# Optimization experiments

Measured on AMD Instinct MI355X. Metric: run time of the kernel, lower is better.

The kernel has to match this reference:

```python
import jax, jax.numpy as jnp
import numpy as np

N_NODES = 100000


def gcn_conv(x, src, dst, W, b, n_nodes):
    """PyG GCNConv: out = D^{-1/2} (A + I) D^{-1/2} (x @ W) + b.
    src/dst are the original (non-self-loop) edges; self loops handled analytically.
    """
    h = x @ W  # [N, out]
    ones = jnp.ones(src.shape[0], dtype=h.dtype)
    # degree including self loop
    deg = jax.ops.segment_sum(ones, dst, num_segments=n_nodes) + 1.0  # [N]
    dinv = jax.lax.rsqrt(deg)
    norm = dinv[src] * dinv[dst]  # [E]
    msg = h[src] * norm[:, None]  # gather + scale
    agg = jax.ops.segment_sum(msg, dst, num_segments=n_nodes)  # scatter-add
    # self-loop contribution: norm = deg^{-1/2} * deg^{-1/2} = 1/deg
    agg = agg + h * (1.0 / deg)[:, None]
    return agg + b


def setup_inputs() -> dict:
    key = jax.random.key(0)
    k1, k2, k3, k4 = jax.random.split(key, 4)
    n, e = N_NODES, 3200000
    x = jax.random.normal(k1, (n, 256), dtype=jnp.float32)
    edge_index = jax.random.randint(k2, (2, e), 0, n, dtype=jnp.int64)
    W1 = jax.random.normal(k3, (256, 64), dtype=jnp.float32) * (1.0 / np.sqrt(256))
    b1 = jnp.zeros((64,), dtype=jnp.float32)
    W2 = jax.random.normal(k4, (64, 4), dtype=jnp.float32) * (1.0 / np.sqrt(64))
    b2 = jnp.zeros((4,), dtype=jnp.float32)
    return {"x": x, "edge_index": edge_index, "W1": W1, "b1": b1, "W2": W2, "b2": b2}


def reference(x, edge_index, W1, b1, W2, b2):
    n = x.shape[0]
    src, dst = edge_index[0], edge_index[1]
    h = gcn_conv(x, src, dst, W1, b1, n)
    h = jax.nn.leaky_relu(h, negative_slope=0.01)  # nn.LeakyReLU default
    # F.dropout in eval mode is identity
    h = gcn_conv(h, src, dst, W2, b2, n)
    return jax.nn.softmax(h, axis=1)
```

## Files before the change

### kernel.cpp

```cpp
#include <hip/hip_runtime.h>
#include <hip/hip_bf16.h>
#include <math.h>


#define NB 512
#define MAXB 512
#define SCHUNK 6400

typedef __attribute__((ext_vector_type(8))) short bf16x8;
typedef __attribute__((ext_vector_type(4))) float f32x4;

__device__ __forceinline__ int edge_val(const void* ep, size_t idx, int is64) {
    if (is64) return (int)(((const long long*)ep)[idx]);
    return ((const int*)ep)[idx];
}

__device__ __forceinline__ unsigned short f2bf(float f) {
    unsigned int u = __float_as_uint(f);
    return (unsigned short)((u + 0x7FFFu + ((u >> 16) & 1u)) >> 16);
}
__device__ __forceinline__ float bf2f(unsigned short b) {
    return __uint_as_float((unsigned int)b << 16);
}

__global__ void detect_width(const unsigned int* __restrict__ ew, int* __restrict__ flag) {
    if (threadIdx.x == 0 && blockIdx.x == 0) {
        int f = 1;
        for (int i = 0; i < 64; ++i)
            if (ew[2 * i + 1] != 0u) { f = 0; break; }
        *flag = f;
    }
}

__global__ __launch_bounds__(256) void hist_pass(
    const void* __restrict__ edges, int E, const int* __restrict__ flagp,
    int* __restrict__ ghist, int B) {
    __shared__ int hist[MAXB];
    const int tid = threadIdx.x;
    for (int i = tid; i < B; i += 256) hist[i] = 0;
    __syncthreads();
    const int is64 = *flagp;
    const int per = (E + NB - 1) / NB;
    const int s0 = blockIdx.x * per;
    const int s1 = min(s0 + per, E);
    for (int i = s0 + tid; i < s1; i += 256) {
        const int d = edge_val(edges, (size_t)E + i, is64);
        atomicAdd(&hist[d >> 8], 1);
    }
    __syncthreads();
    for (int i = tid; i < B; i += 256) ghist[(size_t)blockIdx.x * B + i] = hist[i];
}

__global__ __launch_bounds__(NB) void col_scan(
    const int* __restrict__ ghist, int* __restrict__ goff,
    int* __restrict__ bsum, int B) {
    __shared__ int sm[NB];
    const int tid = threadIdx.x;
    const int b = blockIdx.x;
    const int v = ghist[(size_t)tid * B + b];
    sm[tid] = v;
    __syncthreads();
    for (int off = 1; off < NB; off <<= 1) {
        int val = (tid >= off) ? sm[tid - off] : 0;
        __syncthreads();
        sm[tid] += val;
        __syncthreads();
    }
    goff[(size_t)tid * B + b] = sm[tid] - v;
    if (tid == NB - 1) bsum[b] = sm[tid];
}

__global__ __launch_bounds__(512) void base_scan(
    const int* __restrict__ bsum, int* __restrict__ bbase,
    int* __restrict__ row_ptr, int B, int n, int E) {
    __shared__ int sm[512];
    const int tid = threadIdx.x;
    const int v = (tid < B) ? bsum[tid] : 0;
    sm[tid] = v;
    __syncthreads();
    for (int off = 1; off < 512; off <<= 1) {
        int val = (tid >= off) ? sm[tid - off] : 0;
        __syncthreads();
        sm[tid] += val;
        __syncthreads();
    }
    if (tid < B) bbase[tid] = sm[tid] - v;
    if (tid == 0) { bbase[B] = E; row_ptr[n] = E; }
}

__global__ __launch_bounds__(512) void scatter_pass(
    const void* __restrict__ edges, int E, const int* __restrict__ flagp,
    const int* __restrict__ ghist, const int* __restrict__ goff,
    const int* __restrict__ bbase, unsigned int* __restrict__ ebuf, int B) {
    __shared__ unsigned int buf[SCHUNK];
    __shared__ int lb[MAXB];
    __shared__ int lf[MAXB];
    __shared__ int sm[MAXB];
    const int tid = threadIdx.x;
    const int blk = blockIdx.x;
    const int is64 = *flagp;
    const int per = (E + NB - 1) / NB;
    const int s0 = blk * per;
    const int s1 = min(s0 + per, E);

    if (per <= SCHUNK) {
        const int c = (tid < B) ? ghist[(size_t)blk * B + tid] : 0;
        sm[tid] = c;
        __syncthreads();
        for (int off = 1; off < MAXB; off <<= 1) {
            int val = (tid >= off) ? sm[tid - off] : 0;
            __syncthreads();
            sm[tid] += val;
            __syncthreads();
        }
        if (tid < B) { lb[tid] = sm[tid] - c; lf[tid] = sm[tid] - c; }
        __syncthreads();
        for (int i = s0 + tid; i < s1; i += 512) {
            const int d = edge_val(edges, (size_t)E + i, is64);
            const int s = edge_val(edges, (size_t)i, is64);
            const unsigned int val = ((unsigned int)s << 8) | (unsigned int)(d & 255);
            const int pos = atomicAdd(&lf[d >> 8], 1);
            buf[pos] = val;
        }
        __syncthreads();
        const int lane = tid & 63;
        const int wv = tid >> 6;
        for (int b = wv; b < B; b += 8) {
            const int lo = lb[b];
            const int cnt = lf[b] - lo;
            if (cnt > 0) {
                unsigned int* dst = ebuf + bbase[b] + goff[(size_t)blk * B + b];
                for (int k = lane; k < cnt; k += 64) dst[k] = buf[lo + k];
            }
        }
    } else {
        for (int i = tid; i < B; i += 512)
            lf[i] = bbase[i] + goff[(size_t)blk * B + i];
        __syncthreads();
        for (int i = s0 + tid; i < s1; i += 512) {
            const int d = edge_val(edges, (size_t)E + i, is64);
            const int s = edge_val(edges, (size_t)i, is64);
            const int pos = atomicAdd(&lf[d >> 8], 1);
            ebuf[pos] = ((unsigned int)s << 8) | (unsigned int)(d & 255);
        }
    }
}

__global__ __launch_bounds__(512) void bucket_csr(
    const unsigned int* __restrict__ ebuf, const int* __restrict__ bbase,
    int* __restrict__ row_ptr, float* __restrict__ dinv,
    int* __restrict__ col_src, int n) {
    __shared__ int hist[256];
    __shared__ int scn[256];
    __shared__ int fill[256];
    const int tid = threadIdx.x;
    const int b = blockIdx.x;
    if (tid < 256) hist[tid] = 0;
    __syncthreads();
    const int base = bbase[b];
    const int m = bbase[b + 1] - base;
    const unsigned int* eb = ebuf + base;
    for (int i = tid; i < m; i += 512) atomicAdd(&hist[eb[i] & 255u], 1);
    __syncthreads();
    if (tid < 256) scn[tid] = hist[tid];
    __syncthreads();
    for (int off = 1; off < 256; off <<= 1) {
        int val = 0;
        if (tid < 256 && tid >= off) val = scn[tid - off];
        __syncthreads();
        if (tid < 256) scn[tid] += val;
        __syncthreads();
    }
    if (tid < 256) {
        const int excl = scn[tid] - hist[tid];
        fill[tid] = excl;
        const int v = b * 256 + tid;
        if (v < n) {
            row_ptr[v] = base + excl;
            dinv[v] = rsqrtf((float)hist[tid] + 1.0f);
        }
    }
    __syncthreads();
    for (int i = tid; i < m; i += 512) {
        const unsigned int e = eb[i];
        const int p = atomicAdd(&fill[e & 255u], 1);
        col_src[base + p] = (int)(e >> 8);
    }
}

__global__ __launch_bounds__(256) void gemm1_kernel(
    const float* __restrict__ x, const float* __restrict__ W1,
    const float* __restrict__ dinv, unsigned short* __restrict__ hs1b, int n) {
    __shared__ unsigned short wt[64 * 264];
    const int tid = threadIdx.x;
    for (int i = tid; i < 4096; i += 256) {
        const int k = i >> 4;
        const int c0 = (i & 15) * 4;
        const float4 w = *((const float4*)W1 + i);
        wt[(c0 + 0) * 264 + k] = f2bf(w.x);
        wt[(c0 + 1) * 264 + k] = f2bf(w.y);
        wt[(c0 + 2) * 264 + k] = f2bf(w.z);
        wt[(c0 + 3) * 264 + k] = f2bf(w.w);
    }
    __syncthreads();

    const int lane = tid & 63;
    const int wid = tid >> 6;
    const int row0 = blockIdx.x * 64 + wid * 16;
    const int rr = lane & 15;
    const int kh = lane >> 4;

    union FragU { bf16x8 v; unsigned short u[8]; };
    bf16x8 af[8];
    {
        int r = row0 + rr;
        if (r >= n) r = n - 1;
        const float* xr = x + (size_t)r * 256 + kh * 8;
#pragma unroll
        for (int ks = 0; ks < 8; ++ks) {
            const float4 p0 = *(const float4*)(xr + ks * 32);
            const float4 p1 = *(const float4*)(xr + ks * 32 + 4);
            FragU f;
            f.u[0] = f2bf(p0.x); f.u[1] = f2bf(p0.y);
            f.u[2] = f2bf(p0.z); f.u[3] = f2bf(p0.w);
            f.u[4] = f2bf(p1.x); f.u[5] = f2bf(p1.y);
            f.u[6] = f2bf(p1.z); f.u[7] = f2bf(p1.w);
            af[ks] = f.v;
        }
    }
    f32x4 acc[4];
#pragma unroll
    for (int ct = 0; ct < 4; ++ct) acc[ct] = (f32x4){0.f, 0.f, 0.f, 0.f};
#pragma unroll
    for (int ct = 0; ct < 4; ++ct) {
        const unsigned short* wcol = wt + (ct * 16 + rr) * 264 + kh * 8;
#pragma unroll
        for (int ks = 0; ks < 8; ++ks) {
            const bf16x8 bf = *(const bf16x8*)(wcol + ks * 32);
            acc[ct] = __builtin_amdgcn_mfma_f32_16x16x32_bf16(af[ks], bf, acc[ct], 0, 0, 0);
        }
    }
#pragma unroll
    for (int j = 0; j < 4; ++j) {
        const int gr = row0 + kh * 4 + j;
        if (gr < n) {
            const float dv = dinv[gr];
#pragma unroll
            for (int ct = 0; ct < 4; ++ct)
                hs1b[(size_t)gr * 64 + ct * 16 + rr] = f2bf(acc[ct][j] * dv);
        }
    }
}

__global__ __launch_bounds__(256) void agg1_kernel(
    const int* __restrict__ row_ptr, const int* __restrict__ col_src,
    const unsigned short* __restrict__ hs1b, const float* __restrict__ dinv,
    const float* __restrict__ b1, const float* __restrict__ W2,
    float* __restrict__ hs2, int n) {
    const int lane = threadIdx.x & 63;
    int v = blockIdx.x * 4 + (threadIdx.x >> 6);
    v = __builtin_amdgcn_readfirstlane(v);
    if (v >= n) return;
    const int g = lane >> 4;
    const int q = lane & 15;
    const int rs = row_ptr[v];
    const int re = row_ptr[v + 1];
    float a0 = 0.f, a1 = 0.f, a2 = 0.f, a3 = 0.f;
    float c0 = 0.f, c1 = 0.f, c2 = 0.f, c3 = 0.f;
    int e = rs;
    for (; e + 32 <= re; e += 32) {
        const int cs = col_src[e + (lane & 31)];
        const int s0 = __shfl(cs, 0 + g),  s1 = __shfl(cs, 4 + g);
        const int s2 = __shfl(cs, 8 + g),  s3 = __shfl(cs, 12 + g);
        const int s4 = __shfl(cs, 16 + g), s5 = __shfl(cs, 20 + g);
        const int s6 = __shfl(cs, 24 + g), s7 = __shfl(cs, 28 + g);
        const ushort4 r0 = *((const ushort4*)(hs1b + (size_t)s0 * 64) + q);
        const ushort4 r1 = *((const ushort4*)(hs1b + (size_t)s1 * 64) + q);
        const ushort4 r2 = *((const ushort4*)(hs1b + (size_t)s2 * 64) + q);
        const ushort4 r3 = *((const ushort4*)(hs1b + (size_t)s3 * 64) + q);
        const ushort4 r4 = *((const ushort4*)(hs1b + (size_t)s4 * 64) + q);
        const ushort4 r5 = *((const ushort4*)(hs1b + (size_t)s5 * 64) + q);
        const ushort4 r6 = *((const ushort4*)(hs1b + (size_t)s6 * 64) + q);
        const ushort4 r7 = *((const ushort4*)(hs1b + (size_t)s7 * 64) + q);
        a0 += bf2f(r0.x) + bf2f(r1.x) + bf2f(r2.x) + bf2f(r3.x);
        a1 += bf2f(r0.y) + bf2f(r1.y) + bf2f(r2.y) + bf2f(r3.y);
        a2 += bf2f(r0.z) + bf2f(r1.z) + bf2f(r2.z) + bf2f(r3.z);
        a3 += bf2f(r0.w) + bf2f(r1.w) + bf2f(r2.w) + bf2f(r3.w);
        c0 += bf2f(r4.x) + bf2f(r5.x) + bf2f(r6.x) + bf2f(r7.x);
        c1 += bf2f(r4.y) + bf2f(r5.y) + bf2f(r6.y) + bf2f(r7.y);
        c2 += bf2f(r4.z) + bf2f(r5.z) + bf2f(r6.z) + bf2f(r7.z);
        c3 += bf2f(r4.w) + bf2f(r5.w) + bf2f(r6.w) + bf2f(r7.w);
    }
    a0 += c0; a1 += c1; a2 += c2; a3 += c3;
    for (; e + 16 <= re; e += 16) {
        const int cs = col_src[e + q];
        const int s0 = __shfl(cs, 0 + g);
        const int s1 = __shfl(cs, 4 + g);
        const int s2 = __shfl(cs, 8 + g);
        const int s3 = __shfl(cs, 12 + g);
        const ushort4 r0 = *((const ushort4*)(hs1b + (size_t)s0 * 64) + q);
        const ushort4 r1 = *((const ushort4*)(hs1b + (size_t)s1 * 64) + q);
        const ushort4 r2 = *((const ushort4*)(hs1b + (size_t)s2 * 64) + q);
        const ushort4 r3 = *((const ushort4*)(hs1b + (size_t)s3 * 64) + q);
        a0 += bf2f(r0.x) + bf2f(r1.x) + bf2f(r2.x) + bf2f(r3.x);
        a1 += bf2f(r0.y) + bf2f(r1.y) + bf2f(r2.y) + bf2f(r3.y);
        a2 += bf2f(r0.z) + bf2f(r1.z) + bf2f(r2.z) + bf2f(r3.z);
        a3 += bf2f(r0.w) + bf2f(r1.w) + bf2f(r2.w) + bf2f(r3.w);
    }
    for (; e < re; e += 4) {
        if (e + g < re) {
            const int s = col_src[e + g];
            const ushort4 r = *((const ushort4*)(hs1b + (size_t)s * 64) + q);
            a0 += bf2f(r.x); a1 += bf2f(r.y); a2 += bf2f(r.z); a3 += bf2f(r.w);
        }
    }
    a0 += __shfl_xor(a0, 16); a1 += __shfl_xor(a1, 16);
    a2 += __shfl_xor(a2, 16); a3 += __shfl_xor(a3, 16);
    a0 += __shfl_xor(a0, 32); a1 += __shfl_xor(a1, 32);
    a2 += __shfl_xor(a2, 32); a3 += __shfl_xor(a3, 32);
    const ushort4 sr = *((const ushort4*)(hs1b + (size_t)v * 64) + q);
    const float dv = dinv[v];
    const float4 bb = *((const float4*)b1 + q);
    float4 res;
    res.x = dv * (a0 + bf2f(sr.x)) + bb.x;
    res.y = dv * (a1 + bf2f(sr.y)) + bb.y;
    res.z = dv * (a2 + bf2f(sr.z)) + bb.z;
    res.w = dv * (a3 + bf2f(sr.w)) + bb.w;
    res.x = res.x > 0.f ? res.x : 0.01f * res.x;
    res.y = res.y > 0.f ? res.y : 0.01f * res.y;
    res.z = res.z > 0.f ? res.z : 0.01f * res.z;
    res.w = res.w > 0.f ? res.w : 0.01f * res.w;
    const float4* W2v = (const float4*)W2;
    const float4 w0 = W2v[q * 4 + 0], w1 = W2v[q * 4 + 1];
    const float4 w2 = W2v[q * 4 + 2], w3 = W2v[q * 4 + 3];
    float4 p;
    p.x = res.x * w0.x + res.y * w1.x + res.z * w2.x + res.w * w3.x;
    p.y = res.x * w0.y + res.y * w1.y + res.z * w2.y + res.w * w3.y;
    p.z = res.x * w0.z + res.y * w1.z + res.z * w2.z + res.w * w3.z;
    p.w = res.x * w0.w + res.y * w1.w + res.z * w2.w + res.w * w3.w;
#pragma unroll
    for (int s = 1; s < 16; s <<= 1) {
        p.x += __shfl_xor(p.x, s); p.y += __shfl_xor(p.y, s);
        p.z += __shfl_xor(p.z, s); p.w += __shfl_xor(p.w, s);
    }
    if (lane == 0) {
        float4 o; o.x = p.x * dv; o.y = p.y * dv; o.z = p.z * dv; o.w = p.w * dv;
        *(float4*)(hs2 + (size_t)v * 4) = o;
    }
}

__global__ __launch_bounds__(256) void agg2_kernel(
    const int* __restrict__ row_ptr, const int* __restrict__ col_src,
    const float* __restrict__ hs2, const float* __restrict__ dinv,
    const float* __restrict__ b2, float* __restrict__ out, int n) {
    const int lane = threadIdx.x & 63;
    int v = blockIdx.x * 4 + (threadIdx.x >> 6);
    v = __builtin_amdgcn_readfirstlane(v);
    if (v >= n) return;
    const int c = lane & 3;
    const int ei = lane >> 2;
    const int rs = row_ptr[v];
    const int re = row_ptr[v + 1];
    float acc = 0.f;
    for (int e0 = rs; e0 < re; e0 += 16) {
        const int e = e0 + ei;
        if (e < re) {
            const int s = col_src[e];
            acc += hs2[(size_t)s * 4 + c];
        }
    }
    acc += __shfl_xor(acc, 4);
    acc += __shfl_xor(acc, 8);
    acc += __shfl_xor(acc, 16);
    acc += __shfl_xor(acc, 32);
    const float val = dinv[v] * (acc + hs2[(size_t)v * 4 + c]) + b2[c];
    float m = fmaxf(val, __shfl_xor(val, 1));
    m = fmaxf(m, __shfl_xor(m, 2));
    const float ex = __expf(val - m);
    float s = ex + __shfl_xor(ex, 1);
    s += __shfl_xor(s, 2);
    if (lane < 4) out[(size_t)v * 4 + c] = ex / s;
}

extern "C" void kernel_launch(void* const* d_in, const int* in_sizes, int n_in,
                              void* d_out, int out_size, void* d_ws, size_t ws_size,
                              hipStream_t stream) {
    const float* x  = (const float*)d_in[0];
    const void*  ei = d_in[1];
    const float* W1 = (const float*)d_in[2];
    const float* b1 = (const float*)d_in[3];
    const float* W2 = (const float*)d_in[4];
    const float* b2 = (const float*)d_in[5];
    const int n = in_sizes[0] / 256;
    const int E = in_sizes[1] / 2;
    const int B = (n + 255) / 256;

    char* ws = (char*)d_ws;
    size_t off = 0;
    auto alloc = [&](size_t bytes) -> void* {
        void* p = ws + off;
        off += (bytes + 255) & ~(size_t)255;
        return p;
    };
    int*   flag    = (int*)alloc(sizeof(int) * 64);
    int*   ghist   = (int*)alloc(sizeof(int) * (size_t)NB * B);
    int*   goff    = (int*)alloc(sizeof(int) * (size_t)NB * B);
    int*   bsum    = (int*)alloc(sizeof(int) * B);
    int*   bbase   = (int*)alloc(sizeof(int) * (B + 1));
    int*   row_ptr = (int*)alloc(sizeof(int) * (n + 1));
    int*   col_src = (int*)alloc(sizeof(int) * (size_t)E);
    float* dinv    = (float*)alloc(sizeof(float) * n);
    unsigned short* hs1b = (unsigned short*)alloc(sizeof(unsigned short) * (size_t)n * 64);
    float* hs2     = (float*)alloc(sizeof(float) * (size_t)n * 4);
    unsigned int* ebuf = (unsigned int*)alloc(sizeof(unsigned int) * (size_t)E);
    (void)n_in; (void)out_size; (void)ws_size;

    detect_width<<<1, 64, 0, stream>>>((const unsigned int*)ei, flag);
    hist_pass<<<NB, 256, 0, stream>>>(ei, E, flag, ghist, B);
    col_scan<<<B, NB, 0, stream>>>(ghist, goff, bsum, B);
    base_scan<<<1, 512, 0, stream>>>(bsum, bbase, row_ptr, B, n, E);
    scatter_pass<<<NB, 512, 0, stream>>>(ei, E, flag, ghist, goff, bbase, ebuf, B);
    bucket_csr<<<B, 512, 0, stream>>>(ebuf, bbase, row_ptr, dinv, col_src, n);
    gemm1_kernel<<<(n + 63) / 64, 256, 0, stream>>>(x, W1, dinv, hs1b, n);
    agg1_kernel<<<(n + 3) / 4, 256, 0, stream>>>(row_ptr, col_src, hs1b, dinv, b1, W2, hs2, n);
    agg2_kernel<<<(n + 3) / 4, 256, 0, stream>>>(row_ptr, col_src, hs2, dinv, b2, (float*)d_out, n);
}
```

Measured before the change: 210.5 us.

## Store layer-1 features in FP8 and use 16-lane-per-node aggregation

After: 188.2 us. -10.6%, faster.

```diff
diff --git a/kernel.cpp b/kernel.cpp
--- a/kernel.cpp
+++ b/kernel.cpp
@@ -3,12 +3,13 @@
 #include <math.h>
 
 
-#define NB 512
+#define NB 256
 #define MAXB 512
-#define SCHUNK 6400
+#define SCHUNK 12544
 
 typedef __attribute__((ext_vector_type(8))) short bf16x8;
 typedef __attribute__((ext_vector_type(4))) float f32x4;
+typedef __attribute__((ext_vector_type(2))) float f32x2;
 
 __device__ __forceinline__ int edge_val(const void* ep, size_t idx, int is64) {
     if (is64) return (int)(((const long long*)ep)[idx]);
@@ -19,17 +20,23 @@
     unsigned int u = __float_as_uint(f);
     return (unsigned short)((u + 0x7FFFu + ((u >> 16) & 1u)) >> 16);
 }
-__device__ __forceinline__ float bf2f(unsigned short b) {
-    return __uint_as_float((unsigned int)b << 16);
+
+__device__ __forceinline__ void acc_fp8row(unsigned int r, float& a0, float& a1,
+                                           float& a2, float& a3) {
+    const f32x2 lo = __builtin_amdgcn_cvt_pk_f32_fp8((int)r, false);
+    const f32x2 hi = __builtin_amdgcn_cvt_pk_f32_fp8((int)r, true);
+    a0 += lo[0]; a1 += lo[1]; a2 += hi[0]; a3 += hi[1];
+}
+
+__device__ __forceinline__ unsigned char f32_to_fp8(float f) {
+    const int enc = __builtin_amdgcn_cvt_pk_fp8_f32(f, 0.f, 0, false);
+    return (unsigned char)(enc & 0xff);
 }
 
 __global__ void detect_width(const unsigned int* __restrict__ ew, int* __restrict__ flag) {
-    if (threadIdx.x == 0 && blockIdx.x == 0) {
-        int f = 1;
-        for (int i = 0; i < 64; ++i)
-            if (ew[2 * i + 1] != 0u) { f = 0; break; }
-        *flag = f;
-    }
+    const int i = threadIdx.x;
+    const unsigned long long m = __ballot(ew[2 * i + 1] != 0u);
+    if (i == 0) *flag = (m == 0ull) ? 1 : 0;
 }
 
 __global__ __launch_bounds__(256) void hist_pass(
@@ -190,7 +197,7 @@
 
 __global__ __launch_bounds__(256) void gemm1_kernel(
     const float* __restrict__ x, const float* __restrict__ W1,
-    const float* __restrict__ dinv, unsigned short* __restrict__ hs1b, int n) {
+    const float* __restrict__ dinv, unsigned char* __restrict__ hs1f8, int n) {
     __shared__ unsigned short wt[64 * 264];
     const int tid = threadIdx.x;
     for (int i = tid; i < 4096; i += 256) {
@@ -247,85 +254,53 @@
             const float dv = dinv[gr];
 #pragma unroll
             for (int ct = 0; ct < 4; ++ct)
-                hs1b[(size_t)gr * 64 + ct * 16 + rr] = f2bf(acc[ct][j] * dv);
+                hs1f8[(size_t)gr * 64 + ct * 16 + rr] = f32_to_fp8(acc[ct][j] * dv);
         }
     }
 }
 
 __global__ __launch_bounds__(256) void agg1_kernel(
     const int* __restrict__ row_ptr, const int* __restrict__ col_src,
-    const unsigned short* __restrict__ hs1b, const float* __restrict__ dinv,
+    const unsigned char* __restrict__ hs1f8, const float* __restrict__ dinv,
     const float* __restrict__ b1, const float* __restrict__ W2,
     float* __restrict__ hs2, int n) {
-    const int lane = threadIdx.x & 63;
-    int v = blockIdx.x * 4 + (threadIdx.x >> 6);
-    v = __builtin_amdgcn_readfirstlane(v);
+    const int tid = threadIdx.x;
+    const int q = tid & 15;
+    const int v = blockIdx.x * 16 + (tid >> 4);
     if (v >= n) return;
-    const int g = lane >> 4;
-    const int q = lane & 15;
     const int rs = row_ptr[v];
     const int re = row_ptr[v + 1];
     float a0 = 0.f, a1 = 0.f, a2 = 0.f, a3 = 0.f;
-    float c0 = 0.f, c1 = 0.f, c2 = 0.f, c3 = 0.f;
     int e = rs;
-    for (; e + 32 <= re; e += 32) {
-        const int cs = col_src[e + (lane & 31)];
-        const int s0 = __shfl(cs, 0 + g),  s1 = __shfl(cs, 4 + g);
-        const int s2 = __shfl(cs, 8 + g),  s3 = __shfl(cs, 12 + g);
-        const int s4 = __shfl(cs, 16 + g), s5 = __shfl(cs, 20 + g);
-        const int s6 = __shfl(cs, 24 + g), s7 = __shfl(cs, 28 + g);
-        const ushort4 r0 = *((const ushort4*)(hs1b + (size_t)s0 * 64) + q);
-        const ushort4 r1 = *((const ushort4*)(hs1b + (size_t)s1 * 64) + q);
-        const ushort4 r2 = *((const ushort4*)(hs1b + (size_t)s2 * 64) + q);
-        const ushort4 r3 = *((const ushort4*)(hs1b + (size_t)s3 * 64) + q);
-        const ushort4 r4 = *((const ushort4*)(hs1b + (size_t)s4 * 64) + q);
-        const ushort4 r5 = *((const ushort4*)(hs1b + (size_t)s5 * 64) + q);
-        const ushort4 r6 = *((const ushort4*)(hs1b + (size_t)s6 * 64) + q);
-        const ushort4 r7 = *((const ushort4*)(hs1b + (size_t)s7 * 64) + q);
-        a0 += bf2f(r0.x) + bf2f(r1.x) + bf2f(r2.x) + bf2f(r3.x);
-        a1 += bf2f(r0.y) + bf2f(r1.y) + bf2f(r2.y) + bf2f(r3.y);
-        a2 += bf2f(r0.z) + bf2f(r1.z) + bf2f(r2.z) + bf2f(r3.z);
-        a3 += bf2f(r0.w) + bf2f(r1.w) + bf2f(r2.w) + bf2f(r3.w);
-        c0 += bf2f(r4.x) + bf2f(r5.x) + bf2f(r6.x) + bf2f(r7.x);
-        c1 += bf2f(r4.y) + bf2f(r5.y) + bf2f(r6.y) + bf2f(r7.y);
-        c2 += bf2f(r4.z) + bf2f(r5.z) + bf2f(r6.z) + bf2f(r7.z);
-        c3 += bf2f(r4.w) + bf2f(r5.w) + bf2f(r6.w) + bf2f(r7.w);
-    }
-    a0 += c0; a1 += c1; a2 += c2; a3 += c3;
     for (; e + 16 <= re; e += 16) {
         const int cs = col_src[e + q];
-        const int s0 = __shfl(cs, 0 + g);
-        const int s1 = __shfl(cs, 4 + g);
-        const int s2 = __shfl(cs, 8 + g);
-        const int s3 = __shfl(cs, 12 + g);
-        const ushort4 r0 = *((const ushort4*)(hs1b + (size_t)s0 * 64) + q);
-        const ushort4 r1 = *((const ushort4*)(hs1b + (size_t)s1 * 64) + q);
-        const ushort4 r2 = *((const ushort4*)(hs1b + (size_t)s2 * 64) + q);
-        const ushort4 r3 = *((const ushort4*)(hs1b + (size_t)s3 * 64) + q);
-        a0 += bf2f(r0.x) + bf2f(r1.x) + bf2f(r2.x) + bf2f(r3.x);
-        a1 += bf2f(r0.y) + bf2f(r1.y) + bf2f(r2.y) + bf2f(r3.y);
-        a2 += bf2f(r0.z) + bf2f(r1.z) + bf2f(r2.z) + bf2f(r3.z);
-        a3 += bf2f(r0.w) + bf2f(r1.w) + bf2f(r2.w) + bf2f(r3.w);
-    }
-    for (; e < re; e += 4) {
-        if (e + g < re) {
-            const int s = col_src[e + g];
-            const ushort4 r = *((const ushort4*)(hs1b + (size_t)s * 64) + q);
-            a0 += bf2f(r.x); a1 += bf2f(r.y); a2 += bf2f(r.z); a3 += bf2f(r.w);
-        }
-    }
-    a0 += __shfl_xor(a0, 16); a1 += __shfl_xor(a1, 16);
-    a2 += __shfl_xor(a2, 16); a3 += __shfl_xor(a3, 16);
-    a0 += __shfl_xor(a0, 32); a1 += __shfl_xor(a1, 32);
-    a2 += __shfl_xor(a2, 32); a3 += __shfl_xor(a3, 32);
-    const ushort4 sr = *((const ushort4*)(hs1b + (size_t)v * 64) + q);
+        unsigned int r[16];
+#pragma unroll
+        for (int j = 0; j < 16; ++j) {
+            const int s = __shfl(cs, j, 16);
+            r[j] = *(const unsigned int*)(hs1f8 + (size_t)s * 64 + q * 4);
+        }
+#pragma unroll
+        for (int j = 0; j < 16; ++j) acc_fp8row(r[j], a0, a1, a2, a3);
+    }
+    const int rem = re - e;
+    if (rem > 0) {
+        const int cs = col_src[(q < rem) ? e + q : re - 1];
+        for (int j = 0; j < rem; ++j) {
+            const int s = __shfl(cs, j, 16);
+            const unsigned int r = *(const unsigned int*)(hs1f8 + (size_t)s * 64 + q * 4);
+            acc_fp8row(r, a0, a1, a2, a3);
+        }
+    }
+    float s0 = 0.f, s1 = 0.f, s2 = 0.f, s3 = 0.f;
+    acc_fp8row(*(const unsigned int*)(hs1f8 + (size_t)v * 64 + q * 4), s0, s1, s2, s3);
     const float dv = dinv[v];
-    const float4 bb = *((const float4*)b1 + q);
+    const float4 bb = ((const float4*)b1)[q];
     float4 res;
-    res.x = dv * (a0 + bf2f(sr.x)) + bb.x;
-    res.y = dv * (a1 + bf2f(sr.y)) + bb.y;
-    res.z = dv * (a2 + bf2f(sr.z)) + bb.z;
-    res.w = dv * (a3 + bf2f(sr.w)) + bb.w;
+    res.x = dv * (a0 + s0) + bb.x;
+    res.y = dv * (a1 + s1) + bb.y;
+    res.z = dv * (a2 + s2) + bb.z;
+    res.w = dv * (a3 + s3) + bb.w;
     res.x = res.x > 0.f ? res.x : 0.01f * res.x;
     res.y = res.y > 0.f ? res.y : 0.01f * res.y;
     res.z = res.z > 0.f ? res.z : 0.01f * res.z;
@@ -340,10 +315,10 @@
     p.w = res.x * w0.w + res.y * w1.w + res.z * w2.w + res.w * w3.w;
 #pragma unroll
     for (int s = 1; s < 16; s <<= 1) {
-        p.x += __shfl_xor(p.x, s); p.y += __shfl_xor(p.y, s);
-        p.z += __shfl_xor(p.z, s); p.w += __shfl_xor(p.w, s);
-    }
-    if (lane == 0) {
+        p.x += __shfl_xor(p.x, s, 16); p.y += __shfl_xor(p.y, s, 16);
+        p.z += __shfl_xor(p.z, s, 16); p.w += __shfl_xor(p.w, s, 16);
+    }
+    if (q == 0) {
         float4 o; o.x = p.x * dv; o.y = p.y * dv; o.z = p.z * dv; o.w = p.w * dv;
         *(float4*)(hs2 + (size_t)v * 4) = o;
     }
@@ -410,7 +385,7 @@
     int*   row_ptr = (int*)alloc(sizeof(int) * (n + 1));
     int*   col_src = (int*)alloc(sizeof(int) * (size_t)E);
     float* dinv    = (float*)alloc(sizeof(float) * n);
-    unsigned short* hs1b = (unsigned short*)alloc(sizeof(unsigned short) * (size_t)n * 64);
+    unsigned char* hs1f8 = (unsigned char*)alloc(sizeof(unsigned char) * (size_t)n * 64);
     float* hs2     = (float*)alloc(sizeof(float) * (size_t)n * 4);
     unsigned int* ebuf = (unsigned int*)alloc(sizeof(unsigned int) * (size_t)E);
     (void)n_in; (void)out_size; (void)ws_size;
@@ -421,7 +396,7 @@
     base_scan<<<1, 512, 0, stream>>>(bsum, bbase, row_ptr, B, n, E);
     scatter_pass<<<NB, 512, 0, stream>>>(ei, E, flag, ghist, goff, bbase, ebuf, B);
     bucket_csr<<<B, 512, 0, stream>>>(ebuf, bbase, row_ptr, dinv, col_src, n);
-    gemm1_kernel<<<(n + 63) / 64, 256, 0, stream>>>(x, W1, dinv, hs1b, n);
-    agg1_kernel<<<(n + 3) / 4, 256, 0, stream>>>(row_ptr, col_src, hs1b, dinv, b1, W2, hs2, n);
+    gemm1_kernel<<<(n + 63) / 64, 256, 0, stream>>>(x, W1, dinv, hs1f8, n);
+    agg1_kernel<<<(n + 15) / 16, 256, 0, stream>>>(row_ptr, col_src, hs1f8, dinv, b1, W2, hs2, n);
     agg2_kernel<<<(n + 3) / 4, 256, 0, stream>>>(row_ptr, col_src, hs2, dinv, b2, (float*)d_out, n);
 }
```
